# Optimization experiments

Hardware: AMD Instinct MI355X
Metric: run time of the kernel (lower is better)

The kernel has to match this reference:

```python
import jax, jax.numpy as jnp
import numpy as np

B = 8
SEQ = 8192
D_MODEL = 256
D_STATE = 64
D_CONV = 4
EXPAND = 4
HEADDIM = 64
N_LAYERS = 8
D_INNER = EXPAND * D_MODEL            # 1024
NHEADS = D_INNER // HEADDIM           # 16
CONV_DIM = D_INNER + 2 * D_STATE      # 1152 (ngroups=1)
D_IN_PROJ = 2 * D_INNER + 2 * D_STATE + NHEADS  # 2192


def setup_inputs():
    key = jax.random.key(0)
    ks = jax.random.split(key, 16)
    rn = lambda k, shape, fan: jax.random.normal(k, shape, jnp.float32) / np.float32(np.sqrt(fan))
    inp = {}
    inp["x"] = jax.random.normal(ks[0], (B, 3, SEQ), jnp.float32)
    inp["conv1_w"] = rn(ks[1], (64, 3, 16), 3 * 16)
    inp["conv1_b"] = rn(ks[2], (64,), 64)
    inp["conv2_w"] = rn(ks[3], (D_MODEL, 64, 16), 64 * 16)
    inp["conv2_b"] = rn(ks[4], (D_MODEL,), D_MODEL)
    inp["in_proj_w"] = rn(ks[5], (N_LAYERS, D_IN_PROJ, D_MODEL), D_MODEL)
    inp["dw_conv_w"] = rn(ks[6], (N_LAYERS, CONV_DIM, D_CONV), D_CONV)
    inp["dw_conv_b"] = rn(ks[7], (N_LAYERS, CONV_DIM), D_CONV)
    inp["dt_bias"] = jax.random.normal(ks[8], (N_LAYERS, NHEADS), jnp.float32) * 0.5
    inp["A_log"] = jax.random.uniform(ks[9], (N_LAYERS, NHEADS), jnp.float32, 0.0, 2.0)
    inp["ssm_D"] = jnp.ones((N_LAYERS, NHEADS), jnp.float32)
    inp["rms_w"] = jnp.ones((N_LAYERS, D_INNER), jnp.float32)
    inp["out_proj_w"] = rn(ks[10], (N_LAYERS, D_MODEL, D_INNER), D_INNER)
    inp["ln_w"] = jnp.ones((D_MODEL,), jnp.float32)
    inp["ln_b"] = jnp.zeros((D_MODEL,), jnp.float32)
    inp["reg1_w"] = rn(ks[11], (128, D_MODEL), D_MODEL)
    inp["reg1_b"] = rn(ks[12], (128,), 128)
    inp["reg2_w"] = rn(ks[13], (1, 128), 128)
    inp["reg2_b"] = rn(ks[14], (1,), 128)
    return inp


def _silu(v):
    return v * jax.nn.sigmoid(v)


def _mamba2_layer(u, in_proj_w, dw_w, dw_b, dt_bias, A_log, ssm_D, rms_w, out_proj_w):
    b, l, _ = u.shape
    zxbcdt = u @ in_proj_w.T                               # (b,l,2192)
    z = zxbcdt[..., :D_INNER]
    xBC = zxbcdt[..., D_INNER:D_INNER + CONV_DIM]
    dt = jax.nn.softplus(zxbcdt[..., D_INNER + CONV_DIM:] + dt_bias)   # (b,l,h)
    # causal depthwise conv1d (kernel D_CONV), then SiLU
    pad = jnp.pad(xBC, ((0, 0), (D_CONV - 1, 0), (0, 0)))
    conv = sum(pad[:, k:k + l, :] * dw_w[:, k] for k in range(D_CONV)) + dw_b
    xBC = _silu(conv)
    xh = xBC[..., :D_INNER].reshape(b, l, NHEADS, HEADDIM)  # (b,l,h,p)
    Bm = xBC[..., D_INNER:D_INNER + D_STATE]                # (b,l,n)
    Cm = xBC[..., D_INNER + D_STATE:]                       # (b,l,n)
    dA = jnp.exp(dt * (-jnp.exp(A_log)))                    # (b,l,h)

    def step(h, inp):
        dA_t, dt_t, x_t, B_t, C_t = inp
        h = h * dA_t[:, :, None, None] + (dt_t[:, :, None] * x_t)[..., None] * B_t[:, None, None, :]
        y = jnp.einsum('bhpn,bn->bhp', h, C_t)
        return h, y

    h0 = jnp.zeros((b, NHEADS, HEADDIM, D_STATE), u.dtype)
    xs = (dA.transpose(1, 0, 2), dt.transpose(1, 0, 2),
          xh.transpose(1, 0, 2, 3), Bm.transpose(1, 0, 2), Cm.transpose(1, 0, 2))
    _, ys = jax.lax.scan(step, h0, xs)                      # (l,b,h,p)
    y = ys.transpose(1, 0, 2, 3) + ssm_D[None, None, :, None] * xh
    y = y.reshape(b, l, D_INNER)
    y = y * _silu(z)                                        # gated
    y = y * jax.lax.rsqrt(jnp.mean(y * y, axis=-1, keepdims=True) + 1e-5) * rms_w
    return y @ out_proj_w.T


def reference(x, conv1_w, conv1_b, conv2_w, conv2_b, in_proj_w, dw_conv_w, dw_conv_b,
              dt_bias, A_log, ssm_D, rms_w, out_proj_w, ln_w, ln_b,
              reg1_w, reg1_b, reg2_w, reg2_b):
    dn = ('NCH', 'OIH', 'NCH')
    h = jax.lax.conv_general_dilated(x, conv1_w, (4,), [(6, 6)], dimension_numbers=dn) + conv1_b[None, :, None]
    h = jax.nn.gelu(h, approximate=False)
    h = jax.lax.conv_general_dilated(h, conv2_w, (2,), [(7, 7)], dimension_numbers=dn) + conv2_b[None, :, None]
    h = jax.nn.gelu(h, approximate=False)
    h = h.transpose(0, 2, 1)                                # (b, 1024, d_model)
    for i in range(N_LAYERS):
        h = _mamba2_layer(h, in_proj_w[i], dw_conv_w[i], dw_conv_b[i],
                          dt_bias[i], A_log[i], ssm_D[i], rms_w[i], out_proj_w[i])
    mu = jnp.mean(h, -1, keepdims=True)
    var = jnp.mean((h - mu) ** 2, -1, keepdims=True)
    h = (h - mu) * jax.lax.rsqrt(var + 1e-5) * ln_w + ln_b  # LayerNorm
    pooled = h.mean(1)
    r = jax.nn.gelu(pooled @ reg1_w.T + reg1_b, approximate=False)
    return r @ reg2_w.T + reg2_b                            # (b, 1)
```

## Files before the change

### kernel.cpp

```cpp
#include <hip/hip_runtime.h>
#include <math.h>

#define NB       8
#define SEQ      8192
#define L1OUT    2048
#define LOUT     1024
#define DMODEL   256
#define DINNER   1024
#define NHEADS   16
#define HEADDIM  64
#define DSTATE   64
#define CONVDIM  1152
#define DINPROJ  2192
#define NPADIN   2304
#define NLAYERS  8
#define NCHUNK   16
#define Q        64

#define N_CAST1 (NLAYERS * NPADIN * DMODEL)
#define N_CAST2 (NLAYERS * DMODEL * DINNER)
#define N_CAST3 (DMODEL * 1024)

typedef _Float16 f16;
typedef __attribute__((ext_vector_type(8))) _Float16 f16x8;
typedef __attribute__((ext_vector_type(4))) _Float16 f16x4;
typedef __attribute__((ext_vector_type(4))) float    f32x4;

__device__ __forceinline__ float gelu_f(float v) {
    return 0.5f * v * (1.0f + erff(v * 0.70710678118654752f));
}
__device__ __forceinline__ float silu_f(float v) {
    return v * __builtin_amdgcn_rcpf(1.0f + __expf(-v));
}

__device__ __forceinline__ void gload16(const void* g, void* l) {
    __builtin_amdgcn_global_load_lds(
        (const __attribute__((address_space(1))) unsigned int*)g,
        (__attribute__((address_space(3))) unsigned int*)l, 16, 0, 0);
}

__device__ __forceinline__ int xcd_chunk(int flat, int nblk) {
    return (flat & 7) * (nblk >> 3) + (flat >> 3);
}

__global__ __launch_bounds__(256) void k_castall(const float* __restrict__ w_in,
                                                 const float* __restrict__ w_out,
                                                 const float* __restrict__ w_c2,
                                                 f16* __restrict__ o_in,
                                                 f16* __restrict__ o_out,
                                                 f16* __restrict__ o_c2) {
    int idx = blockIdx.x * 256 + threadIdx.x;
    if (idx < N_CAST1) {
        int c = idx & 255;
        int r = (idx >> 8) % NPADIN;
        int l = idx / (NPADIN * 256);
        float v = (r < DINPROJ) ? w_in[((size_t)l * DINPROJ + r) * 256 + c] : 0.f;
        o_in[idx] = (f16)v;
    } else if (idx < N_CAST1 + N_CAST2) {
        int i = idx - N_CAST1;
        o_out[i] = (f16)w_out[i];
    } else if (idx < N_CAST1 + N_CAST2 + N_CAST3) {
        int i = idx - N_CAST1 - N_CAST2;
        o_c2[i] = (f16)w_c2[i];
    }
}

__global__ __launch_bounds__(256) void k_conv1(const float* __restrict__ x,
                                               const float* __restrict__ w,
                                               const float* __restrict__ bias,
                                               f16* __restrict__ out) {
    int idx = blockIdx.x * 256 + threadIdx.x;
    int u  = idx & 255;
    int co = (idx >> 8) & 63;
    int b  = idx >> 14;
    int xbase = u * 32 - 8;

    float acc[8];
#pragma unroll
    for (int t = 0; t < 8; ++t) acc[t] = bias[co];

#pragma unroll
    for (int ci = 0; ci < 3; ++ci) {
        const float* xp = x + ((size_t)b * 3 + ci) * SEQ;
        float xb[48];
#pragma unroll
        for (int j = 0; j < 12; ++j) {
            int off = xbase + j * 4;
            float4 v;
            if (off >= 0 && off + 3 < SEQ) {
                v = *(const float4*)&xp[off];
            } else {
                v.x = (off + 0 >= 0 && off + 0 < SEQ) ? xp[off + 0] : 0.f;
                v.y = (off + 1 >= 0 && off + 1 < SEQ) ? xp[off + 1] : 0.f;
                v.z = (off + 2 >= 0 && off + 2 < SEQ) ? xp[off + 2] : 0.f;
                v.w = (off + 3 >= 0 && off + 3 < SEQ) ? xp[off + 3] : 0.f;
            }
            xb[j * 4 + 0] = v.x; xb[j * 4 + 1] = v.y;
            xb[j * 4 + 2] = v.z; xb[j * 4 + 3] = v.w;
        }
        const float* wp = w + (co * 3 + ci) * 16;
        float wv[16];
#pragma unroll
        for (int k = 0; k < 16; ++k) wv[k] = wp[k];
#pragma unroll
        for (int t = 0; t < 8; ++t)
#pragma unroll
            for (int k = 0; k < 16; ++k)
                acc[t] = fmaf(xb[t * 4 + k + 2], wv[k], acc[t]);
    }
    f16x8 o;
#pragma unroll
    for (int t = 0; t < 8; ++t) o[t] = (f16)gelu_f(acc[t]);
    *(f16x8*)&out[((size_t)(b * 64 + co)) * L1OUT + u * 8] = o;
}

__global__ __launch_bounds__(256) void k_im2col(const f16* __restrict__ h1,
                                                f16* __restrict__ A) {
    int idx = blockIdx.x * 256 + threadIdx.x;
    int g = idx & 127;
    int row = idx >> 7;
    int t = row & (LOUT - 1);
    int b = row >> 10;
    int ci = g >> 1, k0 = (g & 1) * 8;
    int pos0 = t * 2 + k0 - 7;
    const f16* hp = h1 + ((size_t)(b * 64 + ci)) * L1OUT;
    f16x8 v;
#pragma unroll
    for (int j = 0; j < 8; ++j) {
        int p = pos0 + j;
        v[j] = (p >= 0 && p < L1OUT) ? hp[p] : (f16)0.f;
    }
    *(f16x8*)&A[(size_t)row * 1024 + g * 8] = v;
}

template<int BM, int EPI>
__global__ __launch_bounds__(256) void k_hgemm(const f16* __restrict__ A,
                                               const f16* __restrict__ Bw,
                                               f16* __restrict__ Ch,
                                               int M, int N, int K,
                                               const float* __restrict__ bias,
                                               const float* __restrict__ dt_bias,
                                               const float* __restrict__ A_log,
                                               float* __restrict__ dadt) {
    constexpr int MI = BM / 32;
    __shared__ f16 As[BM * 64];
    __shared__ f16 Bs[128 * 64];
    int tid  = threadIdx.x;
    int lane = tid & 63, wid = tid >> 6;
    int wm = wid >> 1, wn = wid & 1;

    int nbx = gridDim.x;
    int flat = blockIdx.y * nbx + blockIdx.x;
    int logical = xcd_chunk(flat, nbx * gridDim.y);
    int row0 = (logical / nbx) * BM, col0 = (logical % nbx) * 128;
    int lr = lane & 15, kb = lane >> 4;

    f32x4 acc[MI][4];
#pragma unroll
    for (int mi = 0; mi < MI; ++mi)
#pragma unroll
        for (int ni = 0; ni < 4; ++ni)
            acc[mi][ni] = (f32x4){0.f, 0.f, 0.f, 0.f};

    int sr  = tid >> 3;
    int scx = ((tid & 7) ^ (sr & 7)) * 8;
    int rsw = (lr & 7) * 8;

    for (int k0 = 0; k0 < K; k0 += 64) {
        __syncthreads();
#pragma unroll
        for (int is = 0; is < BM / 32; ++is)
            gload16(A + (size_t)(row0 + is * 32 + sr) * K + k0 + scx,
                    &As[is * 2048 + wid * 512]);
#pragma unroll
        for (int is = 0; is < 4; ++is)
            gload16(Bw + (size_t)(col0 + is * 32 + sr) * K + k0 + scx,
                    &Bs[is * 2048 + wid * 512]);
        __syncthreads();

#pragma unroll
        for (int ks = 0; ks < 2; ++ks) {
            int cbase = (ks * 32 + kb * 8) ^ rsw;
            f16x8 a[MI], b[4];
#pragma unroll
            for (int mi = 0; mi < MI; ++mi)
                a[mi] = *reinterpret_cast<const f16x8*>(
                    &As[(wm * (BM / 2) + mi * 16 + lr) * 64 + cbase]);
#pragma unroll
            for (int ni = 0; ni < 4; ++ni)
                b[ni] = *reinterpret_cast<const f16x8*>(
                    &Bs[(wn * 64 + ni * 16 + lr) * 64 + cbase]);
#pragma unroll
            for (int mi = 0; mi < MI; ++mi)
#pragma unroll
                for (int ni = 0; ni < 4; ++ni)
                    acc[mi][ni] = __builtin_amdgcn_mfma_f32_16x16x32_f16(
                        a[mi], b[ni], acc[mi][ni], 0, 0, 0);
        }
    }

#pragma unroll
    for (int mi = 0; mi < MI; ++mi)
#pragma unroll
        for (int ni = 0; ni < 4; ++ni) {
            int ccol = col0 + wn * 64 + ni * 16 + lr;
            if (ccol < N) {
                int rbase = row0 + wm * (BM / 2) + mi * 16 + kb * 4;
                f32x4 v = acc[mi][ni];
#pragma unroll
                for (int r = 0; r < 4; ++r) {
                    float val = v[r];
                    if (EPI == 1) val = gelu_f(val + bias[ccol]);
                    Ch[(size_t)(rbase + r) * N + ccol] = (f16)val;
                    if (EPI == 2 && ccol >= DINNER + CONVDIM) {
                        int hh = ccol - (DINNER + CONVDIM);
                        float raw = val + dt_bias[hh];
                        float dtv = (raw > 20.f) ? raw : log1pf(__expf(raw));
                        float lda = -__expf(A_log[hh]) * dtv;
                        *(float2*)&dadt[(size_t)(rbase + r) * 32 + hh * 2] =
                            make_float2(lda, dtv);
                    }
                }
            }
        }
}

__global__ __launch_bounds__(256) void k_ssd1(const f16* __restrict__ zx16,
                                              const float* __restrict__ dadt,
                                              const float* __restrict__ dw_w,
                                              const float* __restrict__ dw_b,
                                              const float* __restrict__ ssmD,
                                              f16* __restrict__ y1,
                                              f16* __restrict__ Sbuf16,
                                              float* __restrict__ Abuf,
                                              f16* __restrict__ C16) {
    __shared__ f16 Bs[64][72];
    __shared__ f16 Cs[64][72];
    __shared__ float GT[64][68];
    __shared__ f16 Mw[4][64][72];
    __shared__ float2 LaDt[4][64];

    int tid = threadIdx.x, lane = tid & 63, wid = tid >> 6;
    int bid = xcd_chunk(blockIdx.x, NB * NCHUNK * 4);
    int hq = bid & 3, c = (bid >> 2) & 15, b = bid >> 6;
    int h = hq * 4 + wid;
    int lr = lane & 15, kb = lane >> 4;
    f16* Xs = &Mw[0][0][0];

    {
        int sg = tid % 48;
        int ts = tid / 48;
        if (ts < 4) {
            int xc;
            if (sg < 32)      xc = hq * 256 + sg * 8;
            else if (sg < 40) xc = 1024 + (sg - 32) * 8;
            else              xc = 1088 + (sg - 40) * 8;
            int zc = 1024 + xc;
            float4 wv[8];
            float  bv[8];
#pragma unroll
            for (int j = 0; j < 8; ++j) {
                wv[j] = *(const float4*)&dw_w[(xc + j) * 4];
                bv[j] = dw_b[xc + j];
            }
            int l0 = c * 64 + ts * 16;
            const f16* zrow = zx16 + ((size_t)(b * 1024 + l0)) * DINPROJ + zc;
            f16x8 r0, r1, r2, r3;
            f16x8 zz;
#pragma unroll
            for (int j = 0; j < 8; ++j) zz[j] = (f16)0.f;
            r0 = (l0 >= 3) ? *(const f16x8*)(zrow - 3 * DINPROJ) : zz;
            r1 = (l0 >= 2) ? *(const f16x8*)(zrow - 2 * DINPROJ) : zz;
            r2 = (l0 >= 1) ? *(const f16x8*)(zrow - 1 * DINPROJ) : zz;
#pragma unroll
            for (int t = 0; t < 16; ++t) {
                r3 = *(const f16x8*)(zrow + t * DINPROJ);
                f16x8 o;
#pragma unroll
                for (int j = 0; j < 8; ++j) {
                    float s = bv[j];
                    s = fmaf((float)r0[j], wv[j].x, s);
                    s = fmaf((float)r1[j], wv[j].y, s);
                    s = fmaf((float)r2[j], wv[j].z, s);
                    s = fmaf((float)r3[j], wv[j].w, s);
                    o[j] = (f16)silu_f(s);
                }
                int row = ts * 16 + t;
                if (sg < 32) {
                    f16x4 o0 = {o[0], o[1], o[2], o[3]};
                    f16x4 o1 = {o[4], o[5], o[6], o[7]};
                    *(f16x4*)&Xs[row * 260 + sg * 8]     = o0;
                    *(f16x4*)&Xs[row * 260 + sg * 8 + 4] = o1;
                } else if (sg < 40) {
                    *(f16x8*)&Bs[row][(sg - 32) * 8] = o;
                } else {
                    *(f16x8*)&Cs[row][(sg - 40) * 8] = o;
                }
                r0 = r1; r1 = r2; r2 = r3;
            }
        }
    }

    float2 ad = *(const float2*)&dadt[((size_t)(b * 1024 + c * 64 + lane) * 16 + h) * 2];
    float La = ad.x;
#pragma unroll
    for (int o = 1; o < 64; o <<= 1) {
        float v = __shfl_up(La, o);
        if (lane >= o) La += v;
    }
    float dt_own = ad.y;
    float La63 = __shfl(La, 63);
    float w_own = __expf(La63 - La) * dt_own;
    LaDt[wid][lane] = make_float2(La, dt_own);
    float Dh = ssmD[h];
    __syncthreads();

    if (hq == 0) {
        f16* cp = C16 + (((size_t)(b * 16 + c)) << 12);
#pragma unroll
        for (int it = 0; it < 2; ++it) {
            int cid = it * 256 + tid;
            int row = cid >> 3, off = (cid & 7) * 8;
            *(f16x8*)&cp[row * 64 + off] = *(const f16x8*)&Cs[row][off];
        }
    }

    f16x8 xfrag[4][2];
#pragma unroll
    for (int pi = 0; pi < 4; ++pi)
#pragma unroll
        for (int ks = 0; ks < 2; ++ks) {
            f16x8 v;
#pragma unroll
            for (int j = 0; j < 8; ++j)
                v[j] = Xs[(ks * 32 + kb * 8 + j) * 260 + wid * 64 + pi * 16 + lr];
            xfrag[pi][ks] = v;
        }

    {
        int tq = wid & 1, sq = wid >> 1;
        f32x4 g[2][2];
#pragma unroll
        for (int i = 0; i < 2; ++i)
#pragma unroll
            for (int j = 0; j < 2; ++j) g[i][j] = (f32x4){0.f, 0.f, 0.f, 0.f};
#pragma unroll
        for (int ks = 0; ks < 2; ++ks) {
            f16x8 a[2], bb[2];
#pragma unroll
            for (int ti = 0; ti < 2; ++ti)
                a[ti] = *(const f16x8*)&Cs[tq * 32 + ti * 16 + lr][ks * 32 + kb * 8];
#pragma unroll
            for (int si = 0; si < 2; ++si)
                bb[si] = *(const f16x8*)&Bs[sq * 32 + si * 16 + lr][ks * 32 + kb * 8];
#pragma unroll
            for (int ti = 0; ti < 2; ++ti)
#pragma unroll
                for (int si = 0; si < 2; ++si)
                    g[ti][si] = __builtin_amdgcn_mfma_f32_16x16x32_f16(
                        a[ti], bb[si], g[ti][si], 0, 0, 0);
        }
#pragma unroll
        for (int ti = 0; ti < 2; ++ti)
#pragma unroll
            for (int si = 0; si < 2; ++si)
#pragma unroll
                for (int r = 0; r < 4; ++r)
                    GT[sq * 32 + si * 16 + lr][tq * 32 + ti * 16 + kb * 4 + r] = g[ti][si][r];
    }
    __syncthreads();

    {
        f16x8 brow[8];
#pragma unroll
        for (int i = 0; i < 8; ++i) brow[i] = *(const f16x8*)&Bs[lane][i * 8];
#pragma unroll
        for (int i = 0; i < 8; ++i)
#pragma unroll
            for (int j = 0; j < 8; ++j)
                Mw[wid][i * 8 + j][lane] = (f16)((float)brow[i][j] * w_own);
    }
    __builtin_amdgcn_wave_barrier();

    f16x8 sbfrag[4][2];
#pragma unroll
    for (int ni = 0; ni < 4; ++ni)
#pragma unroll
        for (int ks = 0; ks < 2; ++ks)
            sbfrag[ni][ks] = *(const f16x8*)&Mw[wid][ni * 16 + lr][ks * 32 + kb * 8];

    {
        f32x4 accS[4][4];
#pragma unroll
        for (int pi = 0; pi < 4; ++pi)
#pragma unroll
            for (int ni = 0; ni < 4; ++ni) accS[pi][ni] = (f32x4){0.f, 0.f, 0.f, 0.f};
#pragma unroll
        for (int ks = 0; ks < 2; ++ks)
#pragma unroll
            for (int pi = 0; pi < 4; ++pi)
#pragma unroll
                for (int ni = 0; ni < 4; ++ni)
                    accS[pi][ni] = __builtin_amdgcn_mfma_f32_16x16x32_f16(
                        xfrag[pi][ks], sbfrag[ni][ks], accS[pi][ni], 0, 0, 0);
        size_t sbase = ((size_t)((b * 16 + h) * 16 + c)) << 12;
#pragma unroll
        for (int pi = 0; pi < 4; ++pi)
#pragma unroll
            for (int ni = 0; ni < 4; ++ni)
#pragma unroll
                for (int r = 0; r < 4; ++r)
                    Sbuf16[sbase + (size_t)(pi * 16 + kb * 4 + r) * 64 + ni * 16 + lr] =
                        (f16)accS[pi][ni][r];
        if (lane == 0) Abuf[(b * 16 + h) * 16 + c] = __expf(La63);
    }
    __builtin_amdgcn_wave_barrier();

    {
        int t = lane;
        float la_t = La;
#pragma unroll
        for (int s8 = 0; s8 < 8; ++s8) {
            f16x8 mv;
#pragma unroll
            for (int j = 0; j < 8; ++j) {
                int s = s8 * 8 + j;
                float2 ld = LaDt[wid][s];
                float m = (s <= t) ? GT[s][t] * __expf(la_t - ld.x) * ld.y : 0.f;
                if (s == t) m += Dh;
                mv[j] = (f16)m;
            }
            *(f16x8*)&Mw[wid][t][s8 * 8] = mv;
        }
    }
    __builtin_amdgcn_wave_barrier();

    {
        f32x4 accY[4][4];
#pragma unroll
        for (int ti = 0; ti < 4; ++ti)
#pragma unroll
            for (int pi = 0; pi < 4; ++pi) accY[ti][pi] = (f32x4){0.f, 0.f, 0.f, 0.f};
#pragma unroll
        for (int ks = 0; ks < 2; ++ks) {
            f16x8 af[4];
#pragma unroll
            for (int ti = 0; ti < 4; ++ti)
                af[ti] = *(const f16x8*)&Mw[wid][ti * 16 + lr][ks * 32 + kb * 8];
#pragma unroll
            for (int ti = 0; ti < 4; ++ti)
#pragma unroll
                for (int pi = 0; pi < 4; ++pi)
                    accY[ti][pi] = __builtin_amdgcn_mfma_f32_16x16x32_f16(
                        af[ti], xfrag[pi][ks], accY[ti][pi], 0, 0, 0);
        }
        f16* yp = y1 + ((size_t)(b * 1024 + c * 64)) * 1024 + h * 64;
#pragma unroll
        for (int ti = 0; ti < 4; ++ti)
#pragma unroll
            for (int pi = 0; pi < 4; ++pi)
#pragma unroll
                for (int r = 0; r < 4; ++r)
                    yp[(size_t)(ti * 16 + kb * 4 + r) * 1024 + pi * 16 + lr] =
                        (f16)accY[ti][pi][r];
    }
}

__global__ __launch_bounds__(256) void k_ssd2f(const f16* __restrict__ C16,
                                               const f16* __restrict__ Sbuf16,
                                               const float* __restrict__ Abuf,
                                               const float* __restrict__ dadt,
                                               f16* __restrict__ y2) {
    __shared__ f16 Hs[NCHUNK][4096];
    int tid = threadIdx.x, lane = tid & 63, wv = tid >> 6;
    int bh = xcd_chunk(blockIdx.x, NB * NHEADS);
    int h = bh & 15, b = bh >> 4;
    int lr = lane & 15, kb = lane >> 4;
    size_t base = (size_t)bh << 16;

    {
        int off = tid * 16;
        int row = tid >> 2;
        int c0f = (tid & 3) * 16;
        int sw = (row & 7) * 8;
        int d0 = row * 64 + (c0f ^ sw);
        int d1 = row * 64 + ((c0f + 8) ^ sw);
        float Hl[16];
#pragma unroll
        for (int j = 0; j < 16; ++j) Hl[j] = 0.f;
#pragma unroll
        for (int c = 0; c < NCHUNK; ++c) {
            f16x8 o0, o1;
#pragma unroll
            for (int j = 0; j < 8; ++j) { o0[j] = (f16)Hl[j]; o1[j] = (f16)Hl[j + 8]; }
            *(f16x8*)&Hs[c][d0] = o0;
            *(f16x8*)&Hs[c][d1] = o1;
            float A = Abuf[bh * 16 + c];
            f16x8 s0 = *(const f16x8*)&Sbuf16[base + (size_t)c * 4096 + off];
            f16x8 s1 = *(const f16x8*)&Sbuf16[base + (size_t)c * 4096 + off + 8];
#pragma unroll
            for (int j = 0; j < 8; ++j) {
                Hl[j]     = fmaf(Hl[j],     A, (float)s0[j]);
                Hl[j + 8] = fmaf(Hl[j + 8], A, (float)s1[j]);
            }
        }
    }
    __syncthreads();

    const f16* cpb = C16 + ((size_t)b << 16);
#pragma unroll
    for (int i = 0; i < 4; ++i) {
        int c = wv * 4 + i;
        float2 ad = *(const float2*)&dadt[((size_t)(b * 1024 + c * 64 + lane) * 16 + h) * 2];
        float La = ad.x;
#pragma unroll
        for (int o = 1; o < 64; o <<= 1) {
            float v = __shfl_up(La, o);
            if (lane >= o) La += v;
        }

        f16x8 hfrag[4][2];
#pragma unroll
        for (int pi = 0; pi < 4; ++pi)
#pragma unroll
            for (int ks = 0; ks < 2; ++ks) {
                int row = pi * 16 + lr;
                int cf = (ks * 32 + kb * 8) ^ ((row & 7) * 8);
                hfrag[pi][ks] = *(const f16x8*)&Hs[c][row * 64 + cf];
            }

        const f16* cp = cpb + ((size_t)c << 12);
        f32x4 acc[4][4];
#pragma unroll
        for (int ti = 0; ti < 4; ++ti)
#pragma unroll
            for (int pi = 0; pi < 4; ++pi) acc[ti][pi] = (f32x4){0.f, 0.f, 0.f, 0.f};
#pragma unroll
        for (int ks = 0; ks < 2; ++ks) {
            f16x8 af[4];
#pragma unroll
            for (int ti = 0; ti < 4; ++ti)
                af[ti] = *(const f16x8*)(cp + (ti * 16 + lr) * 64 + ks * 32 + kb * 8);
#pragma unroll
            for (int ti = 0; ti < 4; ++ti)
#pragma unroll
                for (int pi = 0; pi < 4; ++pi)
                    acc[ti][pi] = __builtin_amdgcn_mfma_f32_16x16x32_f16(
                        af[ti], hfrag[pi][ks], acc[ti][pi], 0, 0, 0);
        }
        f16* yp = y2 + ((size_t)(b * 1024 + c * 64)) * 1024 + h * 64;
#pragma unroll
        for (int ti = 0; ti < 4; ++ti)
#pragma unroll
            for (int r = 0; r < 4; ++r) {
                int t = ti * 16 + kb * 4 + r;
                float sc = __expf(__shfl(La, t));
#pragma unroll
                for (int pi = 0; pi < 4; ++pi)
                    yp[(size_t)t * 1024 + pi * 16 + lr] = (f16)(sc * acc[ti][pi][r]);
            }
    }
}

__global__ __launch_bounds__(256) void k_gate(const f16* __restrict__ zx16,
                                              const float* __restrict__ rmsw,
                                              const f16* __restrict__ y1,
                                              const f16* __restrict__ y2,
                                              f16* __restrict__ ygate) {
    __shared__ float sh[4];
    int bl = blockIdx.x, tid = threadIdx.x;
    int c = tid * 4;
    f16x4 y1v = *reinterpret_cast<const f16x4*>(&y1[(size_t)bl * DINNER + c]);
    f16x4 y2v = *reinterpret_cast<const f16x4*>(&y2[(size_t)bl * DINNER + c]);
    f16x4 z4  = *reinterpret_cast<const f16x4*>(&zx16[(size_t)bl * DINPROJ + c]);
    float v[4];
    float ss = 0.f;
#pragma unroll
    for (int j = 0; j < 4; ++j) {
        v[j] = ((float)y1v[j] + (float)y2v[j]) * silu_f((float)z4[j]);
        ss += v[j] * v[j];
    }
    int lane = tid & 63, wid = tid >> 6;
#pragma unroll
    for (int o = 32; o > 0; o >>= 1) ss += __shfl_down(ss, o, 64);
    if (lane == 0) sh[wid] = ss;
    __syncthreads();
    float total = sh[0] + sh[1] + sh[2] + sh[3];
    float r = rsqrtf(total * (1.f / DINNER) + 1e-5f);
    f16x4 o4;
    o4.x = (f16)(v[0] * r * rmsw[c + 0]);
    o4.y = (f16)(v[1] * r * rmsw[c + 1]);
    o4.z = (f16)(v[2] * r * rmsw[c + 2]);
    o4.w = (f16)(v[3] * r * rmsw[c + 3]);
    *reinterpret_cast<f16x4*>(&ygate[(size_t)bl * DINNER + c]) = o4;
}

__global__ __launch_bounds__(256) void k_lnpool(const f16* __restrict__ h,
                                                const float* __restrict__ lnw,
                                                const float* __restrict__ lnb,
                                                float* __restrict__ pooledp) {
    __shared__ float pl[4][256];
    int bid = blockIdx.x;
    int b = bid >> 5, seg = bid & 31;
    int tid = threadIdx.x, lane = tid & 63, w = tid >> 6;
    int c4 = lane * 4;
    float4 lw = *(const float4*)&lnw[c4];
    float4 lb = *(const float4*)&lnb[c4];
    float acc0 = 0.f, acc1 = 0.f, acc2 = 0.f, acc3 = 0.f;
    const f16* hb = h + ((size_t)b * 1024 + seg * 32 + w * 8) * DMODEL;
#pragma unroll
    for (int i = 0; i < 8; ++i) {
        f16x4 hv = *(const f16x4*)(hb + (size_t)i * DMODEL + c4);
        float vx = (float)hv.x, vy = (float)hv.y, vz = (float)hv.z, vw = (float)hv.w;
        float s1 = vx + vy + vz + vw;
        float s2 = vx * vx + vy * vy + vz * vz + vw * vw;
#pragma unroll
        for (int o = 32; o > 0; o >>= 1) {
            s1 += __shfl_xor(s1, o);
            s2 += __shfl_xor(s2, o);
        }
        float mu = s1 * (1.f / DMODEL);
        float var = s2 * (1.f / DMODEL) - mu * mu;
        float rr = rsqrtf(var + 1e-5f);
        acc0 += (vx - mu) * rr * lw.x + lb.x;
        acc1 += (vy - mu) * rr * lw.y + lb.y;
        acc2 += (vz - mu) * rr * lw.z + lb.z;
        acc3 += (vw - mu) * rr * lw.w + lb.w;
    }
    pl[w][c4 + 0] = acc0; pl[w][c4 + 1] = acc1;
    pl[w][c4 + 2] = acc2; pl[w][c4 + 3] = acc3;
    __syncthreads();
    float tot = pl[0][tid] + pl[1][tid] + pl[2][tid] + pl[3][tid];
    pooledp[(size_t)(b * 32 + seg) * 256 + tid] = tot;
}

__global__ __launch_bounds__(128) void k_head(const float* __restrict__ pooledp,
                                              const float* __restrict__ w1,
                                              const float* __restrict__ b1,
                                              const float* __restrict__ w2,
                                              const float* __restrict__ b2,
                                              float* __restrict__ out) {
    __shared__ float sp[256];
    __shared__ float red[2];
    int b = blockIdx.x, j = threadIdx.x;
    for (int d = j; d < 256; d += 128) {
        float s = 0.f;
#pragma unroll
        for (int seg = 0; seg < 32; ++seg)
            s += pooledp[(size_t)(b * 32 + seg) * 256 + d];
        sp[d] = s * (1.f / LOUT);
    }
    __syncthreads();
    float acc = b1[j];
#pragma unroll 8
    for (int d = 0; d < DMODEL; ++d)
        acc = fmaf(sp[d], w1[j * DMODEL + d], acc);
    float r = gelu_f(acc) * w2[j];
#pragma unroll
    for (int o = 32; o > 0; o >>= 1) r += __shfl_down(r, o, 64);
    int lane = j & 63, wid = j >> 6;
    if (lane == 0) red[wid] = r;
    __syncthreads();
    if (j == 0) out[b] = red[0] + red[1] + b2[0];
}

extern "C" void kernel_launch(void* const* d_in, const int* in_sizes, int n_in,
                              void* d_out, int out_size, void* d_ws, size_t ws_size,
                              hipStream_t stream) {
    const float* x         = (const float*)d_in[0];
    const float* conv1_w   = (const float*)d_in[1];
    const float* conv1_b   = (const float*)d_in[2];
    const float* conv2_w   = (const float*)d_in[3];
    const float* conv2_b   = (const float*)d_in[4];
    const float* in_proj_w = (const float*)d_in[5];
    const float* dw_w      = (const float*)d_in[6];
    const float* dw_b      = (const float*)d_in[7];
    const float* dt_bias   = (const float*)d_in[8];
    const float* A_log     = (const float*)d_in[9];
    const float* ssm_D     = (const float*)d_in[10];
    const float* rms_w     = (const float*)d_in[11];
    const float* out_proj_w= (const float*)d_in[12];
    const float* ln_w      = (const float*)d_in[13];
    const float* ln_b      = (const float*)d_in[14];
    const float* reg1_w    = (const float*)d_in[15];
    const float* reg1_b    = (const float*)d_in[16];
    const float* reg2_w    = (const float*)d_in[17];
    const float* reg2_b    = (const float*)d_in[18];

    float* ws = (float*)d_ws;
    size_t off = 0;
    float* dadt    = ws + off; off += (size_t)NB * LOUT * NHEADS * 2;
    float* Abuf    = ws + off; off += (size_t)NB * NHEADS * NCHUNK;
    float* pooledp = ws + off; off += (size_t)NB * 32 * 256;

    f16* fbase = (f16*)(ws + off);
    size_t foff = 0;
    f16* c1f16  = fbase + foff; foff += (size_t)NB * 64 * L1OUT;
    f16* hbf0   = fbase + foff; foff += (size_t)NB * LOUT * DMODEL;
    f16* hbf1   = fbase + foff; foff += (size_t)NB * LOUT * DMODEL;
    f16* ygate  = fbase + foff; foff += (size_t)NB * LOUT * DINNER;
    f16* y2     = fbase + foff; foff += (size_t)NB * LOUT * DINNER;
    f16* y1     = fbase + foff; foff += (size_t)NB * LOUT * DINNER;
    f16* C16    = fbase + foff; foff += (size_t)NB * NCHUNK * 64 * 64;
    f16* zx16   = fbase + foff; foff += (size_t)NB * LOUT * DINPROJ;
    f16* Sbuf16 = fbase + foff; foff += (size_t)NB * NHEADS * NCHUNK * 4096;
    f16* w_in_h = fbase + foff; foff += (size_t)NLAYERS * NPADIN * DMODEL;
    f16* w_out_h= fbase + foff; foff += (size_t)NLAYERS * DMODEL * DINNER;
    f16* w_c2_h = fbase + foff; foff += (size_t)DMODEL * 1024;
    f16* im2h   = y1;

    {
        int total = N_CAST1 + N_CAST2 + N_CAST3;
        k_castall<<<(total + 255) / 256, 256, 0, stream>>>(
            in_proj_w, out_proj_w, conv2_w, w_in_h, w_out_h, w_c2_h);
    }

    k_conv1<<<(NB * 64 * 256) / 256, 256, 0, stream>>>(x, conv1_w, conv1_b, c1f16);
    k_im2col<<<(NB * LOUT * 128) / 256, 256, 0, stream>>>(c1f16, im2h);
    {
        dim3 g(256 / 128, 8192 / 64);
        k_hgemm<64, 1><<<g, 256, 0, stream>>>(im2h, w_c2_h, hbf0,
                                              8192, 256, 1024, conv2_b,
                                              nullptr, nullptr, nullptr);
    }

    f16* hcur = hbf0;
    f16* hnxt = hbf1;
    for (int i = 0; i < NLAYERS; ++i) {
        {
            dim3 g(NPADIN / 128, 8192 / 128);
            k_hgemm<128, 2><<<g, 256, 0, stream>>>(
                hcur, w_in_h + (size_t)i * NPADIN * DMODEL, zx16,
                8192, DINPROJ, DMODEL, nullptr,
                dt_bias + i * NHEADS, A_log + i * NHEADS, dadt);
        }
        k_ssd1<<<NB * NCHUNK * 4, 256, 0, stream>>>(
            zx16, dadt, dw_w + (size_t)i * CONVDIM * 4, dw_b + (size_t)i * CONVDIM,
            ssm_D + i * NHEADS, y1, Sbuf16, Abuf, C16);
        k_ssd2f<<<NB * NHEADS, 256, 0, stream>>>(C16, Sbuf16, Abuf, dadt, y2);
        k_gate<<<NB * LOUT, 256, 0, stream>>>(zx16, rms_w + (size_t)i * DINNER,
                                              y1, y2, ygate);
        {
            dim3 g(DMODEL / 128, 8192 / 64);
            k_hgemm<64, 0><<<g, 256, 0, stream>>>(
                ygate, w_out_h + (size_t)i * DMODEL * DINNER, hnxt,
                8192, DMODEL, DINNER, nullptr, nullptr, nullptr, nullptr);
        }
        f16* tmp = hcur; hcur = hnxt; hnxt = tmp;
    }

    k_lnpool<<<NB * 32, 256, 0, stream>>>(hcur, ln_w, ln_b, pooledp);
    k_head<<<NB, 128, 0, stream>>>(pooledp, reg1_w, reg1_b, reg2_w, reg2_b, (float*)d_out);
}
```

Measured before the change: 849.4 us.

## Split SSD state-pass kernel across headdim quarters and give each gate row one wave

The inter-chunk SSD kernel now launches four blocks per (batch, head), each handling a 16-wide slice of the head dimension. This raises the grid from 128 to 512 blocks, improving occupancy across CUs and shrinking shared memory per block. The cost is that C and the cumulative decay scan are reloaded and recomputed redundantly by every block. Separately, the gating/RMSNorm kernel now processes one row per wavefront with 16-element vector loads and a shuffle-xor reduction, removing the shared-memory barrier and cutting the block count by four.

```diff
diff --git a/kernel.cpp b/kernel.cpp
--- a/kernel.cpp
+++ b/kernel.cpp
@@ -471,38 +471,32 @@
                                                const float* __restrict__ Abuf,
                                                const float* __restrict__ dadt,
                                                f16* __restrict__ y2) {
-    __shared__ f16 Hs[NCHUNK][4096];
+    __shared__ f16 Hs[NCHUNK][1024];
     int tid = threadIdx.x, lane = tid & 63, wv = tid >> 6;
-    int bh = xcd_chunk(blockIdx.x, NB * NHEADS);
-    int h = bh & 15, b = bh >> 4;
+    int bid = xcd_chunk(blockIdx.x, NB * NHEADS * 4);
+    int ph = bid & 3, h = (bid >> 2) & 15, b = bid >> 6;
+    int bh = b * 16 + h;
     int lr = lane & 15, kb = lane >> 4;
-    size_t base = (size_t)bh << 16;
-
-    {
-        int off = tid * 16;
-        int row = tid >> 2;
-        int c0f = (tid & 3) * 16;
-        int sw = (row & 7) * 8;
-        int d0 = row * 64 + (c0f ^ sw);
-        int d1 = row * 64 + ((c0f + 8) ^ sw);
-        float Hl[16];
-#pragma unroll
-        for (int j = 0; j < 16; ++j) Hl[j] = 0.f;
+    size_t base = ((size_t)bh << 16) + ph * 1024;
+
+    {
+        int lp = tid >> 4;
+        int n0 = (tid & 15) * 4;
+        int dst = lp * 64 + ((((n0 >> 3) ^ (lp & 7))) << 3) + (n0 & 7);
+        float Hl[4];
+#pragma unroll
+        for (int j = 0; j < 4; ++j) Hl[j] = 0.f;
 #pragma unroll
         for (int c = 0; c < NCHUNK; ++c) {
-            f16x8 o0, o1;
-#pragma unroll
-            for (int j = 0; j < 8; ++j) { o0[j] = (f16)Hl[j]; o1[j] = (f16)Hl[j + 8]; }
-            *(f16x8*)&Hs[c][d0] = o0;
-            *(f16x8*)&Hs[c][d1] = o1;
+            f16x4 o;
+#pragma unroll
+            for (int j = 0; j < 4; ++j) o[j] = (f16)Hl[j];
+            *(f16x4*)&Hs[c][dst] = o;
             float A = Abuf[bh * 16 + c];
-            f16x8 s0 = *(const f16x8*)&Sbuf16[base + (size_t)c * 4096 + off];
-            f16x8 s1 = *(const f16x8*)&Sbuf16[base + (size_t)c * 4096 + off + 8];
-#pragma unroll
-            for (int j = 0; j < 8; ++j) {
-                Hl[j]     = fmaf(Hl[j],     A, (float)s0[j]);
-                Hl[j + 8] = fmaf(Hl[j + 8], A, (float)s1[j]);
-            }
+            f16x4 s = *(const f16x4*)&Sbuf16[base + (size_t)c * 4096 + lp * 64 + n0];
+#pragma unroll
+            for (int j = 0; j < 4; ++j)
+                Hl[j] = fmaf(Hl[j], A, (float)s[j]);
         }
     }
     __syncthreads();
@@ -519,22 +513,17 @@
             if (lane >= o) La += v;
         }
 
-        f16x8 hfrag[4][2];
-#pragma unroll
-        for (int pi = 0; pi < 4; ++pi)
-#pragma unroll
-            for (int ks = 0; ks < 2; ++ks) {
-                int row = pi * 16 + lr;
-                int cf = (ks * 32 + kb * 8) ^ ((row & 7) * 8);
-                hfrag[pi][ks] = *(const f16x8*)&Hs[c][row * 64 + cf];
-            }
+        f16x8 hfrag[2];
+#pragma unroll
+        for (int ks = 0; ks < 2; ++ks) {
+            int cf = (ks * 32 + kb * 8) ^ ((lr & 7) * 8);
+            hfrag[ks] = *(const f16x8*)&Hs[c][lr * 64 + cf];
+        }
 
         const f16* cp = cpb + ((size_t)c << 12);
-        f32x4 acc[4][4];
-#pragma unroll
-        for (int ti = 0; ti < 4; ++ti)
-#pragma unroll
-            for (int pi = 0; pi < 4; ++pi) acc[ti][pi] = (f32x4){0.f, 0.f, 0.f, 0.f};
+        f32x4 acc[4];
+#pragma unroll
+        for (int ti = 0; ti < 4; ++ti) acc[ti] = (f32x4){0.f, 0.f, 0.f, 0.f};
 #pragma unroll
         for (int ks = 0; ks < 2; ++ks) {
             f16x8 af[4];
@@ -543,21 +532,17 @@
                 af[ti] = *(const f16x8*)(cp + (ti * 16 + lr) * 64 + ks * 32 + kb * 8);
 #pragma unroll
             for (int ti = 0; ti < 4; ++ti)
-#pragma unroll
-                for (int pi = 0; pi < 4; ++pi)
-                    acc[ti][pi] = __builtin_amdgcn_mfma_f32_16x16x32_f16(
-                        af[ti], hfrag[pi][ks], acc[ti][pi], 0, 0, 0);
-        }
-        f16* yp = y2 + ((size_t)(b * 1024 + c * 64)) * 1024 + h * 64;
+                acc[ti] = __builtin_amdgcn_mfma_f32_16x16x32_f16(
+                    af[ti], hfrag[ks], acc[ti], 0, 0, 0);
+        }
+        f16* yp = y2 + ((size_t)(b * 1024 + c * 64)) * 1024 + h * 64 + ph * 16;
 #pragma unroll
         for (int ti = 0; ti < 4; ++ti)
 #pragma unroll
             for (int r = 0; r < 4; ++r) {
                 int t = ti * 16 + kb * 4 + r;
                 float sc = __expf(__shfl(La, t));
-#pragma unroll
-                for (int pi = 0; pi < 4; ++pi)
-                    yp[(size_t)t * 1024 + pi * 16 + lr] = (f16)(sc * acc[ti][pi][r]);
+                yp[(size_t)t * 1024 + lr] = (f16)(sc * acc[ti][r]);
             }
     }
 }
@@ -567,32 +552,37 @@
                                               const f16* __restrict__ y1,
                                               const f16* __restrict__ y2,
                                               f16* __restrict__ ygate) {
-    __shared__ float sh[4];
-    int bl = blockIdx.x, tid = threadIdx.x;
-    int c = tid * 4;
-    f16x4 y1v = *reinterpret_cast<const f16x4*>(&y1[(size_t)bl * DINNER + c]);
-    f16x4 y2v = *reinterpret_cast<const f16x4*>(&y2[(size_t)bl * DINNER + c]);
-    f16x4 z4  = *reinterpret_cast<const f16x4*>(&zx16[(size_t)bl * DINPROJ + c]);
-    float v[4];
+    int tid = threadIdx.x, lane = tid & 63, w = tid >> 6;
+    int bl = blockIdx.x * 4 + w;
+    int c = lane * 16;
+    const f16* p1 = y1 + (size_t)bl * DINNER + c;
+    const f16* p2 = y2 + (size_t)bl * DINNER + c;
+    const f16* pz = zx16 + (size_t)bl * DINPROJ + c;
+    float v[16];
     float ss = 0.f;
 #pragma unroll
-    for (int j = 0; j < 4; ++j) {
-        v[j] = ((float)y1v[j] + (float)y2v[j]) * silu_f((float)z4[j]);
-        ss += v[j] * v[j];
-    }
-    int lane = tid & 63, wid = tid >> 6;
-#pragma unroll
-    for (int o = 32; o > 0; o >>= 1) ss += __shfl_down(ss, o, 64);
-    if (lane == 0) sh[wid] = ss;
-    __syncthreads();
-    float total = sh[0] + sh[1] + sh[2] + sh[3];
-    float r = rsqrtf(total * (1.f / DINNER) + 1e-5f);
-    f16x4 o4;
-    o4.x = (f16)(v[0] * r * rmsw[c + 0]);
-    o4.y = (f16)(v[1] * r * rmsw[c + 1]);
-    o4.z = (f16)(v[2] * r * rmsw[c + 2]);
-    o4.w = (f16)(v[3] * r * rmsw[c + 3]);
-    *reinterpret_cast<f16x4*>(&ygate[(size_t)bl * DINNER + c]) = o4;
+    for (int hh = 0; hh < 2; ++hh) {
+        f16x8 a = *(const f16x8*)(p1 + hh * 8);
+        f16x8 b2 = *(const f16x8*)(p2 + hh * 8);
+        f16x8 z = *(const f16x8*)(pz + hh * 8);
+#pragma unroll
+        for (int j = 0; j < 8; ++j) {
+            float vv = ((float)a[j] + (float)b2[j]) * silu_f((float)z[j]);
+            v[hh * 8 + j] = vv;
+            ss += vv * vv;
+        }
+    }
+#pragma unroll
+    for (int o = 32; o > 0; o >>= 1) ss += __shfl_xor(ss, o);
+    float r = rsqrtf(ss * (1.f / DINNER) + 1e-5f);
+#pragma unroll
+    for (int hh = 0; hh < 2; ++hh) {
+        f16x8 o8;
+#pragma unroll
+        for (int j = 0; j < 8; ++j)
+            o8[j] = (f16)(v[hh * 8 + j] * r * rmsw[c + hh * 8 + j]);
+        *(f16x8*)&ygate[(size_t)bl * DINNER + c + hh * 8] = o8;
+    }
 }
 
 __global__ __launch_bounds__(256) void k_lnpool(const f16* __restrict__ h,
@@ -737,9 +727,9 @@
         k_ssd1<<<NB * NCHUNK * 4, 256, 0, stream>>>(
             zx16, dadt, dw_w + (size_t)i * CONVDIM * 4, dw_b + (size_t)i * CONVDIM,
             ssm_D + i * NHEADS, y1, Sbuf16, Abuf, C16);
-        k_ssd2f<<<NB * NHEADS, 256, 0, stream>>>(C16, Sbuf16, Abuf, dadt, y2);
-        k_gate<<<NB * LOUT, 256, 0, stream>>>(zx16, rms_w + (size_t)i * DINNER,
-                                              y1, y2, ygate);
+        k_ssd2f<<<NB * NHEADS * 4, 256, 0, stream>>>(C16, Sbuf16, Abuf, dadt, y2);
+        k_gate<<<NB * LOUT / 4, 256, 0, stream>>>(zx16, rms_w + (size_t)i * DINNER,
+                                                  y1, y2, ygate);
         {
             dim3 g(DMODEL / 128, 8192 / 64);
             k_hgemm<64, 0><<<g, 256, 0, stream>>>(
```

After: 856.4 us. No clear change (+0.8%).
